# Optimization experiments

Hardware: AMD Instinct MI355X
Metric: run time of the kernel (lower is better)

Reference implementation:

```python
import jax, jax.numpy as jnp
import numpy as np

NUM_HEAD = 16
D = 1024
HEAD_DIM = D // NUM_HEAD
EPS = 1e-5


def setup_inputs() -> dict:
    key = jax.random.key(0)
    ks = jax.random.split(key, 7)
    B, S = 2, 2048
    s = 1.0 / np.sqrt(D)
    return {
        "x": jax.random.normal(ks[0], (B, S, D), dtype=jnp.float32),
        "wq": jax.random.uniform(ks[1], (D, D), jnp.float32, -s, s),
        "bq": jax.random.uniform(ks[2], (D,), jnp.float32, -s, s),
        "wk": jax.random.uniform(ks[3], (D, D), jnp.float32, -s, s),
        "bk": jax.random.uniform(ks[4], (D,), jnp.float32, -s, s),
        "wv": jax.random.uniform(ks[5], (D, D), jnp.float32, -s, s),
        "bv": jax.random.uniform(ks[6], (D,), jnp.float32, -s, s),
        "gamma": jnp.ones((D,), jnp.float32),
        "beta": jnp.zeros((D,), jnp.float32),
    }


def reference(x, wq, bq, wk, bk, wv, bv, gamma, beta):
    B, S, Dm = x.shape
    # Linear: x @ W^T + b (torch convention), then split heads -> [B, H, S, hd]
    def proj(w, b):
        y = jnp.einsum("bsd,ed->bse", x, w) + b
        return y.reshape(B, S, NUM_HEAD, HEAD_DIM).transpose(0, 2, 1, 3)

    q = proj(wq, bq)
    k = proj(wk, bk)
    v = proj(wv, bv)

    scores = jnp.einsum("bhqd,bhkd->bhqk", q, k) / np.sqrt(HEAD_DIM).astype(x.dtype)
    attn = jax.nn.softmax(scores, axis=-1)
    out = jnp.einsum("bhqk,bhkd->bhqd", attn, v)
    out = out.transpose(0, 2, 1, 3).reshape(B, S, Dm)

    out = out + x
    mu = jnp.mean(out, axis=-1, keepdims=True)
    var = jnp.var(out, axis=-1, keepdims=True)
    out = (out - mu) * jax.lax.rsqrt(var + EPS) * gamma + beta
    return out
```

## Files before the change

### kernel.cpp

```cpp
#include <hip/hip_runtime.h>

typedef unsigned short u16;
typedef unsigned int   u32;
typedef __bf16 bf16x8 __attribute__((ext_vector_type(8)));
typedef float  f32x4  __attribute__((ext_vector_type(4)));

#define D_MODEL 1024
#define SEQ     2048
#define NHEAD   16
#define HD      64
#define SOFTMAX_SCL 0.18033688011112042f

__device__ __forceinline__ u16 f2bf(float f) {
    u32 u;
    __builtin_memcpy(&u, &f, 4);
    u32 r = (u + 0x7fffu + ((u >> 16) & 1u)) >> 16;
    return (u16)r;
}
__device__ __forceinline__ float bf2f(u16 v) {
    u32 u = ((u32)v) << 16;
    float f;
    __builtin_memcpy(&f, &u, 4);
    return f;
}

__device__ __forceinline__ void async_copy16(const u16* g, u16* l) {
    __builtin_amdgcn_global_load_lds(
        (__attribute__((address_space(1))) void*)g,
        (__attribute__((address_space(3))) void*)l, 16, 0, 0);
}

__device__ __forceinline__ uint2 pack4(float a, float b, float c, float d) {
    uint2 r;
    r.x = (u32)f2bf(a) | ((u32)f2bf(b) << 16);
    r.y = (u32)f2bf(c) | ((u32)f2bf(d) << 16);
    return r;
}

#define NX4 ((2 * SEQ * D_MODEL) / 4)
#define NW4 ((D_MODEL * D_MODEL) / 4)
__global__ __launch_bounds__(256) void conv_all(
    const float* __restrict__ x,  const float* __restrict__ wq,
    const float* __restrict__ wk, const float* __restrict__ wv,
    u16* __restrict__ xb, u16* __restrict__ wqb,
    u16* __restrict__ wkb, u16* __restrict__ wvb)
{
    int i = blockIdx.x * 256 + threadIdx.x;
    const float* src; u16* dst; int off;
    if (i < NX4)            { src = x;  dst = xb;  off = i; }
    else if (i < NX4 + NW4) { src = wq; dst = wqb; off = i - NX4; }
    else if (i < NX4 + 2 * NW4) { src = wk; dst = wkb; off = i - NX4 - NW4; }
    else                    { src = wv; dst = wvb; off = i - NX4 - 2 * NW4; }
    float4 a = ((const float4*)src)[off];
    ushort4 o;
    o.x = f2bf(a.x); o.y = f2bf(a.y); o.z = f2bf(a.z); o.w = f2bf(a.w);
    ((ushort4*)dst)[off] = o;
}

__global__ __launch_bounds__(256) void qkv_gemm(
    const u16* __restrict__ xb,
    const u16* __restrict__ wqb, const float* __restrict__ bq,
    const u16* __restrict__ wkb, const float* __restrict__ bk,
    const u16* __restrict__ wvb, const float* __restrict__ bv,
    u16* __restrict__ qb, u16* __restrict__ kb, u16* __restrict__ vt)
{
    const int bid  = blockIdx.x;
    const int pair = bid % 24;
    const int by   = bid / 24;
    const int z    = pair >> 3;
    const int bx   = pair & 7;

    const u16* Ap; const u16* Bp;
    int m0, n0;
    if (z < 2) {
        Ap = (z == 1) ? wkb : wqb;  Bp = xb;
        m0 = bx * 128;
        n0 = by * 128;
    } else {
        Ap = xb;  Bp = wvb;
        m0 = by * 128;
        n0 = bx * 128;
    }

    __shared__ u16 As[128 * 64];
    __shared__ u16 Bs[128 * 64];

    const int tid  = threadIdx.x;
    const int wave = tid >> 6;
    const int lane = tid & 63;
    const int quad = lane >> 4;
    const int l16  = lane & 15;
    const int wm   = wave >> 1;
    const int wn   = wave & 1;
    const int swz  = l16 & 7;

    int rr[4], co[4];
#pragma unroll
    for (int t = 0; t < 4; ++t) {
        int ch = (wave * 4 + t) * 64 + lane;
        rr[t] = ch >> 3;
        co[t] = ((ch & 7) ^ (rr[t] & 7)) * 8;
    }

    f32x4 acc[4][4] = {};

    for (int kt = 0; kt < D_MODEL; kt += 64) {
        __syncthreads();
#pragma unroll
        for (int t = 0; t < 4; ++t) {
            int chbase = (wave * 4 + t) * 64;
            async_copy16(Ap + (size_t)(m0 + rr[t]) * D_MODEL + kt + co[t], As + chbase * 8);
            async_copy16(Bp + (size_t)(n0 + rr[t]) * D_MODEL + kt + co[t], Bs + chbase * 8);
        }
        __syncthreads();

#pragma unroll
        for (int kc = 0; kc < 2; ++kc) {
            bf16x8 af[4], bf_[4];
#pragma unroll
            for (int i = 0; i < 4; ++i)
                af[i] = *(const bf16x8*)&As[(wm * 64 + i * 16 + l16) * 64 + (((kc * 4 + quad) ^ swz) << 3)];
#pragma unroll
            for (int j = 0; j < 4; ++j)
                bf_[j] = *(const bf16x8*)&Bs[(wn * 64 + j * 16 + l16) * 64 + (((kc * 4 + quad) ^ swz) << 3)];
#pragma unroll
            for (int i = 0; i < 4; ++i)
#pragma unroll
                for (int j = 0; j < 4; ++j)
                    acc[i][j] = __builtin_amdgcn_mfma_f32_16x16x32_bf16(af[i], bf_[j], acc[i][j], 0, 0, 0);
        }
    }

    if (z < 2) {
        const int chunk_lo = (quad & 1) * 4;
        u16* out = (z == 1) ? kb : qb;
        const float* bi = (z == 1) ? bk : bq;
        const float scl = (z == 1) ? 1.0f : SOFTMAX_SCL;
        const int fblk = m0 + wm * 64;
#pragma unroll
        for (int i = 0; i < 4; ++i) {
            const int fb = fblk + i * 16 + quad * 4;
            float4 b4 = *(const float4*)&bi[fb];
            const int chunk = i * 2 + (quad >> 1);
#pragma unroll
            for (int j = 0; j < 4; ++j) {
                int token = n0 + wn * 64 + j * 16 + l16;
                uint2 pk = pack4((acc[i][j][0] + b4.x) * scl,
                                 (acc[i][j][1] + b4.y) * scl,
                                 (acc[i][j][2] + b4.z) * scl,
                                 (acc[i][j][3] + b4.w) * scl);
                size_t addr = (size_t)token * D_MODEL + fblk
                            + ((chunk ^ (token & 7)) << 3) + chunk_lo;
                *(uint2*)&out[addr] = pk;
            }
        }
    } else {
#pragma unroll
        for (int j = 0; j < 4; ++j) {
            int feat = n0 + wn * 64 + j * 16 + l16;
            float bias = bv[feat];
            int hh = feat >> 6, d = feat & 63;
            const size_t rowbase = ((size_t)hh * HD + d) * SEQ;
            const int chunk = (quad >> 1) * 4 + 0;
#pragma unroll
            for (int i = 0; i < 4; ++i) {
                int tok = m0 + wm * 64 + i * 16 + quad * 4;
                int b = tok >> 11, s = tok & 2047;
                const int nchunk = (i >> 1) * 4 + quad;
                const int nlo    = (i & 1) * 4;
                uint2 pk = pack4(acc[i][j][0] + bias, acc[i][j][1] + bias,
                                 acc[i][j][2] + bias, acc[i][j][3] + bias);
                size_t addr = (size_t)b * NHEAD * HD * SEQ + rowbase
                            + (s & ~63) + ((nchunk ^ (d & 7)) << 3) + nlo;
                *(uint2*)&vt[addr] = pk;
            }
        }
    }
}

__global__ __launch_bounds__(256) void attn_kernel(
    const u16* __restrict__ qb, const u16* __restrict__ kb, const u16* __restrict__ vtg,
    u16* __restrict__ abp, float* __restrict__ lsums)
{
    const int bid  = blockIdx.x;
    const int bh   = bid & 31;
    const int b    = bh >> 4;
    const int h    = bh & 15;
    const int q0   = ((bid >> 5) & 15) * 128;
    const int half = bid >> 9;

    const int tid  = threadIdx.x;
    const int wave = tid >> 6;
    const int lane = tid & 63;
    const int quad = lane >> 4;
    const int l16  = lane & 15;
    const int swz  = l16 & 7;

    __shared__ u16 Ks[2 * 4096];
    __shared__ u16 Vt[2 * 4096];

    const size_t kbase = (size_t)b * SEQ * D_MODEL + h * 64;
    const size_t vbase = (size_t)(b * NHEAD + h) * HD * SEQ;

    bf16x8 aq[2][2];
#pragma unroll
    for (int rb = 0; rb < 2; ++rb) {
        const int qrow = q0 + wave * 32 + rb * 16 + l16;
        const u16* qrp = qb + (size_t)qrow * D_MODEL + h * 64;
        aq[rb][0] = *(const bf16x8*)(qrp + ((quad ^ swz) << 3));
        aq[rb][1] = *(const bf16x8*)(qrp + (((4 + quad) ^ swz) << 3));
    }

    const int r0 = tid >> 3, r1 = (tid + 256) >> 3;
    const int cs8 = (tid & 7) * 8;
    const u16* kg0 = kb + kbase + (size_t)(half * 1024 + r0) * D_MODEL + cs8;
    const u16* kg1 = kb + kbase + (size_t)(half * 1024 + r1) * D_MODEL + cs8;
    const u16* vg0 = vtg + vbase + (size_t)r0 * SEQ + half * 1024 + cs8;
    const u16* vg1 = vtg + vbase + (size_t)r1 * SEQ + half * 1024 + cs8;
    const int wofs = wave * 512;

    f32x4 oacc[2][4] = {};
    float lsum[2] = {};

    async_copy16(kg0, Ks + wofs);
    async_copy16(kg1, Ks + 2048 + wofs);
    async_copy16(vg0, Vt + wofs);
    async_copy16(vg1, Vt + 2048 + wofs);
    kg0 += 64 * D_MODEL; kg1 += 64 * D_MODEL;
    vg0 += 64;           vg1 += 64;

    for (int t = 0; t < 16; ++t) {
        const int cur = (t & 1) << 12;
        const int nxt = cur ^ 4096;

        __builtin_amdgcn_s_barrier();
        if (t < 15) {
            async_copy16(kg0, Ks + nxt + wofs);
            async_copy16(kg1, Ks + nxt + 2048 + wofs);
            async_copy16(vg0, Vt + nxt + wofs);
            async_copy16(vg1, Vt + nxt + 2048 + wofs);
            kg0 += 64 * D_MODEL; kg1 += 64 * D_MODEL;
            vg0 += 64;           vg1 += 64;
            asm volatile("s_waitcnt vmcnt(4)" ::: "memory");
        } else {
            asm volatile("s_waitcnt vmcnt(0)" ::: "memory");
        }
        __builtin_amdgcn_s_barrier();

        const u16* Kc = Ks + cur;
        const u16* Vc = Vt + cur;

        f32x4 sacc[2][4] = {};
#pragma unroll
        for (int c = 0; c < 2; ++c) {
            bf16x8 bk_[4];
#pragma unroll
            for (int nb = 0; nb < 4; ++nb)
                bk_[nb] = *(const bf16x8*)&Kc[(nb * 16 + l16) * 64 + (((c * 4 + quad) ^ swz) << 3)];
            __builtin_amdgcn_s_setprio(1);
#pragma unroll
            for (int rb = 0; rb < 2; ++rb)
#pragma unroll
                for (int nb = 0; nb < 4; ++nb)
                    sacc[rb][nb] = __builtin_amdgcn_mfma_f32_16x16x32_bf16(bk_[nb], aq[rb][c], sacc[rb][nb], 0, 0, 0);
            __builtin_amdgcn_s_setprio(0);
        }

        bf16x8 ap[2][2];
#pragma unroll
        for (int rb = 0; rb < 2; ++rb) {
            u32 w[4][2];
#pragma unroll
            for (int nb = 0; nb < 4; ++nb) {
                float e0 = exp2f(sacc[rb][nb][0]);
                float e1 = exp2f(sacc[rb][nb][1]);
                float e2 = exp2f(sacc[rb][nb][2]);
                float e3 = exp2f(sacc[rb][nb][3]);
                lsum[rb] += (e0 + e1) + (e2 + e3);
                u32 b0, b1, b2, b3;
                __builtin_memcpy(&b0, &e0, 4); __builtin_memcpy(&b1, &e1, 4);
                __builtin_memcpy(&b2, &e2, 4); __builtin_memcpy(&b3, &e3, 4);
                w[nb][0] = __builtin_amdgcn_perm(b1, b0, 0x07060302);
                w[nb][1] = __builtin_amdgcn_perm(b3, b2, 0x07060302);
            }
            union { u32 d[4]; bf16x8 v; } u0, u1;
            u0.d[0] = w[0][0]; u0.d[1] = w[0][1]; u0.d[2] = w[1][0]; u0.d[3] = w[1][1];
            u1.d[0] = w[2][0]; u1.d[1] = w[2][1]; u1.d[2] = w[3][0]; u1.d[3] = w[3][1];
            ap[rb][0] = u0.v;
            ap[rb][1] = u1.v;
        }

#pragma unroll
        for (int c = 0; c < 2; ++c) {
            bf16x8 bv_[4];
#pragma unroll
            for (int nb = 0; nb < 4; ++nb)
                bv_[nb] = *(const bf16x8*)&Vc[(nb * 16 + l16) * 64 + (((c * 4 + quad) ^ swz) << 3)];
            __builtin_amdgcn_s_setprio(1);
#pragma unroll
            for (int rb = 0; rb < 2; ++rb)
#pragma unroll
                for (int nb = 0; nb < 4; ++nb)
                    oacc[rb][nb] = __builtin_amdgcn_mfma_f32_16x16x32_bf16(ap[rb][c], bv_[nb], oacc[rb][nb], 0, 0, 0);
            __builtin_amdgcn_s_setprio(0);
        }
    }

#pragma unroll
    for (int rb = 0; rb < 2; ++rb) {
        float s = lsum[rb];
        s += __shfl_xor(s, 16, 64);
        s += __shfl_xor(s, 32, 64);
        if (lane < 16)
            lsums[((size_t)bh * 2 + half) * SEQ + q0 + wave * 32 + rb * 16 + lane] = s;
#pragma unroll
        for (int r = 0; r < 4; ++r) {
            int row = q0 + wave * 32 + rb * 16 + quad * 4 + r;
#pragma unroll
            for (int nb = 0; nb < 4; ++nb) {
                int d = nb * 16 + l16;
                abp[(size_t)half * SEQ * 2 * D_MODEL
                    + ((size_t)b * SEQ + row) * D_MODEL + h * 64 + d] = f2bf(oacc[rb][nb][r]);
            }
        }
    }
}

__global__ __launch_bounds__(256) void add_ln(
    const u16* __restrict__ abp, const float* __restrict__ lsums,
    const float* __restrict__ x,
    const float* __restrict__ gamma, const float* __restrict__ beta,
    float* __restrict__ out)
{
    const int row = blockIdx.x;
    const int tid = threadIdx.x;
    const size_t rb = (size_t)row * D_MODEL;
    const int b = row >> 11, s = row & 2047;
    const int h = tid >> 4;
    const int bh = b * NHEAD + h;

    float l = lsums[(size_t)bh * 2 * SEQ + s] + lsums[((size_t)bh * 2 + 1) * SEQ + s];
    float inv = 1.0f / l;

    uint2 a0 = ((const uint2*)(abp + rb))[tid];
    uint2 a1 = ((const uint2*)(abp + (size_t)SEQ * 2 * D_MODEL + rb))[tid];
    float4 xb = ((const float4*)(x + rb))[tid];

    float v[4];
    v[0] = (bf2f((u16)(a0.x & 0xffff)) + bf2f((u16)(a1.x & 0xffff))) * inv + xb.x;
    v[1] = (bf2f((u16)(a0.x >> 16))    + bf2f((u16)(a1.x >> 16)))    * inv + xb.y;
    v[2] = (bf2f((u16)(a0.y & 0xffff)) + bf2f((u16)(a1.y & 0xffff))) * inv + xb.z;
    v[3] = (bf2f((u16)(a0.y >> 16))    + bf2f((u16)(a1.y >> 16)))    * inv + xb.w;

    float sm  = v[0] + v[1] + v[2] + v[3];
    float s2 = v[0]*v[0] + v[1]*v[1] + v[2]*v[2] + v[3]*v[3];
#pragma unroll
    for (int off = 1; off < 64; off <<= 1) {
        sm += __shfl_xor(sm, off, 64);
        s2 += __shfl_xor(s2, off, 64);
    }

    __shared__ float red[2][4];
    int wave = tid >> 6, lane = tid & 63;
    if (lane == 0) { red[0][wave] = sm; red[1][wave] = s2; }
    __syncthreads();
    float st  = red[0][0] + red[0][1] + red[0][2] + red[0][3];
    float s2t = red[1][0] + red[1][1] + red[1][2] + red[1][3];

    float mu   = st * (1.0f / D_MODEL);
    float var  = s2t * (1.0f / D_MODEL) - mu * mu;
    float rstd = rsqrtf(var + 1e-5f);

    float4 g  = ((const float4*)(gamma))[tid];
    float4 bt = ((const float4*)(beta))[tid];
    float4 o;
    o.x = (v[0] - mu) * rstd * g.x + bt.x;
    o.y = (v[1] - mu) * rstd * g.y + bt.y;
    o.z = (v[2] - mu) * rstd * g.z + bt.z;
    o.w = (v[3] - mu) * rstd * g.w + bt.w;
    ((float4*)(out + rb))[tid] = o;
}

extern "C" void kernel_launch(void* const* d_in, const int* in_sizes, int n_in,
                              void* d_out, int out_size, void* d_ws, size_t ws_size,
                              hipStream_t stream) {
    const float* x     = (const float*)d_in[0];
    const float* wq    = (const float*)d_in[1];
    const float* bq    = (const float*)d_in[2];
    const float* wk    = (const float*)d_in[3];
    const float* bk    = (const float*)d_in[4];
    const float* wv    = (const float*)d_in[5];
    const float* bv    = (const float*)d_in[6];
    const float* gamma = (const float*)d_in[7];
    const float* beta  = (const float*)d_in[8];
    float* outp = (float*)d_out;

    char* ws = (char*)d_ws;
    u16*   xb    = (u16*)(ws);
    u16*   wqb   = (u16*)(ws + ((size_t)8  << 20));
    u16*   wkb   = (u16*)(ws + ((size_t)10 << 20));
    u16*   wvb   = (u16*)(ws + ((size_t)12 << 20));
    u16*   qb    = (u16*)(ws + ((size_t)16 << 20));
    u16*   kb    = (u16*)(ws + ((size_t)24 << 20));
    u16*   vt    = (u16*)(ws + ((size_t)32 << 20));
    u16*   abp   = (u16*)(ws + ((size_t)40 << 20));
    float* lsums = (float*)(ws + ((size_t)56 << 20));

    conv_all<<<dim3((NX4 + 3 * NW4) / 256), 256, 0, stream>>>(
        x, wq, wk, wv, xb, wqb, wkb, wvb);
    qkv_gemm<<<dim3(24 * 32), 256, 0, stream>>>(xb, wqb, bq, wkb, bk, wvb, bv, qb, kb, vt);
    attn_kernel<<<dim3(1024), 256, 0, stream>>>(qb, kb, vt, abp, lsums);
    add_ln<<<dim3(2 * SEQ), 256, 0, stream>>>(abp, lsums, x, gamma, beta, outp);
}
```

Before: 195.9 us.

## Double-buffer QKV projection GEMM LDS tiles with async prefetch and BK=32

Reworks the QKV projection GEMM main loop to use two LDS buffers with a K-step of 32. The next tile is prefetched asynchronously while MFMAs run on the current one, and partial vmcnt waits replace the full sync pairs. The LDS layout is re-swizzled so two rows share a 64-element line, and s_setprio is raised around the MFMA block. This aims to hide global load latency behind compute. The cost is twice as many loop iterations and barriers, plus more delicate synchronisation.

```diff
diff --git a/kernel.cpp b/kernel.cpp
--- a/kernel.cpp
+++ b/kernel.cpp
@@ -82,8 +82,8 @@
         n0 = bx * 128;
     }
 
-    __shared__ u16 As[128 * 64];
-    __shared__ u16 Bs[128 * 64];
+    __shared__ u16 As[2 * 4096];
+    __shared__ u16 Bs[2 * 4096];
 
     const int tid  = threadIdx.x;
     const int wave = tid >> 6;
@@ -92,43 +92,59 @@
     const int l16  = lane & 15;
     const int wm   = wave >> 1;
     const int wn   = wave & 1;
-    const int swz  = l16 & 7;
-
-    int rr[4], co[4];
-#pragma unroll
-    for (int t = 0; t < 4; ++t) {
-        int ch = (wave * 4 + t) * 64 + lane;
-        rr[t] = ch >> 3;
-        co[t] = ((ch & 7) ^ (rr[t] & 7)) * 8;
-    }
+
+    const int L0   = tid >> 3;
+    const int pu0  = (tid & 7) ^ (L0 & 7);
+    const int row0 = 2 * L0 + (pu0 >> 2);
+    const int c0   = (pu0 & 3) * 8;
+    const u16* Ag = Ap + (size_t)(m0 + row0) * D_MODEL + c0;
+    const u16* Bg = Bp + (size_t)(n0 + row0) * D_MODEL + c0;
+
+    const int lsub = l16 >> 1;
+    const int prd  = ((((l16 & 1) << 2) | quad) ^ lsub) << 3;
+    const int aline0 = wm * 32 * 64;
+    const int bline0 = wn * 32 * 64;
 
     f32x4 acc[4][4] = {};
 
-    for (int kt = 0; kt < D_MODEL; kt += 64) {
-        __syncthreads();
-#pragma unroll
-        for (int t = 0; t < 4; ++t) {
-            int chbase = (wave * 4 + t) * 64;
-            async_copy16(Ap + (size_t)(m0 + rr[t]) * D_MODEL + kt + co[t], As + chbase * 8);
-            async_copy16(Bp + (size_t)(n0 + rr[t]) * D_MODEL + kt + co[t], Bs + chbase * 8);
-        }
-        __syncthreads();
-
-#pragma unroll
-        for (int kc = 0; kc < 2; ++kc) {
-            bf16x8 af[4], bf_[4];
-#pragma unroll
-            for (int i = 0; i < 4; ++i)
-                af[i] = *(const bf16x8*)&As[(wm * 64 + i * 16 + l16) * 64 + (((kc * 4 + quad) ^ swz) << 3)];
+    async_copy16(Ag, As + tid * 8);
+    async_copy16(Ag + (size_t)64 * D_MODEL, As + 2048 + tid * 8);
+    async_copy16(Bg, Bs + tid * 8);
+    async_copy16(Bg + (size_t)64 * D_MODEL, Bs + 2048 + tid * 8);
+
+    for (int it = 0; it < 32; ++it) {
+        const int cur = (it & 1) << 12;
+        const int nxt = cur ^ 4096;
+
+        __builtin_amdgcn_s_barrier();
+        if (it < 31) {
+            const int kt = (it + 1) * 32;
+            async_copy16(Ag + kt, As + nxt + tid * 8);
+            async_copy16(Ag + kt + (size_t)64 * D_MODEL, As + nxt + 2048 + tid * 8);
+            async_copy16(Bg + kt, Bs + nxt + tid * 8);
+            async_copy16(Bg + kt + (size_t)64 * D_MODEL, Bs + nxt + 2048 + tid * 8);
+            asm volatile("s_waitcnt vmcnt(4)" ::: "memory");
+        } else {
+            asm volatile("s_waitcnt vmcnt(0)" ::: "memory");
+        }
+        __builtin_amdgcn_s_barrier();
+
+        const u16* Ac = As + cur;
+        const u16* Bc = Bs + cur;
+        bf16x8 af[4], bf_[4];
+#pragma unroll
+        for (int i = 0; i < 4; ++i)
+            af[i] = *(const bf16x8*)&Ac[aline0 + (i * 8 + lsub) * 64 + prd];
+#pragma unroll
+        for (int j = 0; j < 4; ++j)
+            bf_[j] = *(const bf16x8*)&Bc[bline0 + (j * 8 + lsub) * 64 + prd];
+        __builtin_amdgcn_s_setprio(1);
+#pragma unroll
+        for (int i = 0; i < 4; ++i)
 #pragma unroll
             for (int j = 0; j < 4; ++j)
-                bf_[j] = *(const bf16x8*)&Bs[(wn * 64 + j * 16 + l16) * 64 + (((kc * 4 + quad) ^ swz) << 3)];
-#pragma unroll
-            for (int i = 0; i < 4; ++i)
-#pragma unroll
-                for (int j = 0; j < 4; ++j)
-                    acc[i][j] = __builtin_amdgcn_mfma_f32_16x16x32_bf16(af[i], bf_[j], acc[i][j], 0, 0, 0);
-        }
+                acc[i][j] = __builtin_amdgcn_mfma_f32_16x16x32_bf16(af[i], bf_[j], acc[i][j], 0, 0, 0);
+        __builtin_amdgcn_s_setprio(0);
     }
 
     if (z < 2) {
@@ -161,7 +177,6 @@
             float bias = bv[feat];
             int hh = feat >> 6, d = feat & 63;
             const size_t rowbase = ((size_t)hh * HD + d) * SEQ;
-            const int chunk = (quad >> 1) * 4 + 0;
 #pragma unroll
             for (int i = 0; i < 4; ++i) {
                 int tok = m0 + wm * 64 + i * 16 + quad * 4;
```

Result: slower. 203.1 us (+3.7%).
